# Performance work log

Hardware: AMD Instinct MI355X
Metric: run time of the kernel (lower is better)

## Reference

```python
import jax, jax.numpy as jnp
import numpy as np

N_NODES = 50000
N_EDGES = 800000
LEAKY_SLOPE = 0.25


def setup_inputs() -> dict:
    key = jax.random.key(0)
    ks = jax.random.split(key, 12)
    in_dim, h = 512, [256, 256, 128, 128]
    x = jax.random.normal(ks[0], (N_NODES, in_dim), dtype=jnp.float32)
    row = jax.random.randint(ks[1], (N_EDGES,), 0, N_NODES, dtype=jnp.int32)
    col = jax.random.randint(ks[2], (N_EDGES,), 0, N_NODES, dtype=jnp.int32)
    vals = jax.random.uniform(ks[3], (N_EDGES,), dtype=jnp.float32)
    def xavier(k, fan_in, fan_out):
        std = np.sqrt(2.0 / (fan_in + fan_out))
        return jax.random.normal(k, (fan_in, fan_out), dtype=jnp.float32) * std
    W1 = xavier(ks[4], in_dim, h[0]); b1 = jnp.zeros((h[0],), jnp.float32)
    W2 = xavier(ks[5], h[0], h[1]);  b2 = jnp.zeros((h[1],), jnp.float32)
    W3 = xavier(ks[6], h[1], h[2]);  b3 = jnp.zeros((h[2],), jnp.float32)
    W4 = xavier(ks[7], h[2], h[3]);  b4 = jnp.zeros((h[3],), jnp.float32)
    return {"x": x, "row": row, "col": col, "vals": vals,
            "W1": W1, "b1": b1, "W2": W2, "b2": b2,
            "W3": W3, "b3": b3, "W4": W4, "b4": b4}


def _gconv(x, row, col, vals, W, b):
    # support = x @ W  (dense transform), then SpMM: out[i] = sum_e vals[e] * support[col[e]] for row[e]==i
    support = x @ W
    msgs = support[col] * vals[:, None]           # [E, out_dim] gather + edge-weight
    out = jax.ops.segment_sum(msgs, row, num_segments=x.shape[0])  # scatter-add
    return out + b


def reference(x, row, col, vals, W1, b1, W2, b2, W3, b3, W4, b4):
    lrelu = lambda t: jnp.where(t >= 0, t, LEAKY_SLOPE * t)
    # dropout is identity in eval mode (deterministic reference)
    h = lrelu(_gconv(x, row, col, vals, W1, b1))
    h = lrelu(_gconv(h, row, col, vals, W2, b2))
    h = lrelu(_gconv(h, row, col, vals, W3, b3))
    h = lrelu(_gconv(h, row, col, vals, W4, b4))
    return h
```

## Files before the change

kernel.cpp:

```cpp
#include <hip/hip_runtime.h>
#include <hip/hip_bf16.h>

#define NN 50000
#define NE 800000
#define LEAKY 0.25f
#define SCAN_NB ((NN + 255) / 256)

typedef __attribute__((ext_vector_type(8))) short bf16x8;
typedef __attribute__((ext_vector_type(8))) ushort u16x8;
typedef __attribute__((ext_vector_type(4))) float f32x4;
typedef unsigned long long ull;

#define AS1 const __attribute__((address_space(1))) void*
#define AS3 __attribute__((address_space(3))) void*

static __device__ __forceinline__ ushort f2bf(float f) {
    union { __hip_bfloat16 h; ushort u; } cv;
    cv.h = __float2bfloat16(f);
    return cv.u;
}
static __device__ __forceinline__ float bf2f(ushort u) {
    union { unsigned u; float f; } cv;
    cv.u = ((unsigned)u) << 16;
    return cv.f;
}

__global__ void cast_bf16_x8(const float4* __restrict__ in, u16x8* __restrict__ out, int n8) {
    int i = blockIdx.x * blockDim.x + threadIdx.x;
    if (i >= n8) return;
    float4 v0 = in[i * 2];
    float4 v1 = in[i * 2 + 1];
    u16x8 o;
    o[0] = f2bf(v0.x); o[1] = f2bf(v0.y); o[2] = f2bf(v0.z); o[3] = f2bf(v0.w);
    o[4] = f2bf(v1.x); o[5] = f2bf(v1.y); o[6] = f2bf(v1.z); o[7] = f2bf(v1.w);
    out[i] = o;
}

__global__ void cast_transpose_all(const float* __restrict__ W1, const float* __restrict__ W2,
                                   const float* __restrict__ W3, const float* __restrict__ W4,
                                   ushort* __restrict__ Wt1, ushort* __restrict__ Wt2,
                                   ushort* __restrict__ Wt3, ushort* __restrict__ Wt4) {
    int idx = blockIdx.x * blockDim.x + threadIdx.x;
    const float* W; ushort* Wt; int K, N, base;
    if (idx < 131072)      { W = W1; Wt = Wt1; K = 512; N = 256; base = 0; }
    else if (idx < 196608) { W = W2; Wt = Wt2; K = 256; N = 256; base = 131072; }
    else if (idx < 229376) { W = W3; Wt = Wt3; K = 256; N = 128; base = 196608; }
    else if (idx < 245760) { W = W4; Wt = Wt4; K = 128; N = 128; base = 229376; }
    else return;
    int l = idx - base;
    int k = l / N, n = l % N;
    Wt[n * K + k] = f2bf(W[l]);
}

template<int BN>
__global__ __launch_bounds__(256) void gemm_bf16(
    const ushort* __restrict__ A, const ushort* __restrict__ Bt,
    ushort* __restrict__ C, int M, int K)
{
    constexpr int NI = BN / 32;
    constexpr int BPASS = BN / 64;
    constexpr int ASZ = 64 * 32;
    constexpr int BSZ = BN * 32;
    __shared__ ushort As[2 * ASZ];
    __shared__ ushort Bs[2 * BSZ];
    const int tid  = threadIdx.x;
    const int lane = tid & 63;
    const int wid  = tid >> 6;
    const int wr = wid >> 1, wc = wid & 1;
    const int m0 = blockIdx.x * 64;

    int ar = m0 + (tid >> 2); if (ar >= M) ar = M - 1;
    const int ccol = (tid & 3) * 8;

    const ushort* gA = A + (size_t)ar * K + ccol;
    const ushort* gB[BPASS];
    #pragma unroll
    for (int p = 0; p < BPASS; ++p)
        gB[p] = Bt + (size_t)(p * 64 + (tid >> 2)) * K + ccol;

    const int fr = lane & 15;
    const int fq = lane >> 4;

    auto STAGE = [&](int buf, int k0) {
        char* lA = (char*)(As + buf * ASZ) + wid * 1024;
        char* lB = (char*)(Bs + buf * BSZ) + wid * 1024;
        __builtin_amdgcn_global_load_lds((AS1)(gA + k0), (AS3)lA, 16, 0, 0);
        #pragma unroll
        for (int p = 0; p < BPASS; ++p)
            __builtin_amdgcn_global_load_lds((AS1)(gB[p] + k0), (AS3)(lB + p * 4096), 16, 0, 0);
    };

    f32x4 acc[2][NI];
    #pragma unroll
    for (int i = 0; i < 2; ++i)
        #pragma unroll
        for (int j = 0; j < NI; ++j)
            acc[i][j] = {0.f, 0.f, 0.f, 0.f};

    STAGE(0, 0);
    const int nk = K >> 5;
    for (int t = 0; t < nk; ++t) {
        const int cur = t & 1;
        __syncthreads();
        if (t + 1 < nk) STAGE(cur ^ 1, (t + 1) << 5);

        const ushort* fragA = As + cur * ASZ + (wr * 32 + fr) * 32 + fq * 8;
        const ushort* fragB = Bs + cur * BSZ + (wc * (BN / 2) + fr) * 32 + fq * 8;
        bf16x8 a[2], b[NI];
        #pragma unroll
        for (int mi = 0; mi < 2; ++mi) a[mi] = *(const bf16x8*)(fragA + mi * 16 * 32);
        #pragma unroll
        for (int ni = 0; ni < NI; ++ni) b[ni] = *(const bf16x8*)(fragB + ni * 16 * 32);
        #pragma unroll
        for (int mi = 0; mi < 2; ++mi)
            #pragma unroll
            for (int ni = 0; ni < NI; ++ni)
                acc[mi][ni] = __builtin_amdgcn_mfma_f32_16x16x32_bf16(a[mi], b[ni], acc[mi][ni], 0, 0, 0);
    }

    #pragma unroll
    for (int mi = 0; mi < 2; ++mi) {
        #pragma unroll
        for (int j = 0; j < 4; ++j) {
            int row = m0 + wr * 32 + mi * 16 + fq * 4 + j;
            if (row >= M) continue;
            #pragma unroll
            for (int ni = 0; ni < NI; ++ni) {
                int colg = wc * (BN / 2) + ni * 16 + fr;
                C[(size_t)row * BN + colg] = f2bf(acc[mi][ni][j]);
            }
        }
    }
}

__global__ void hist_rows(const int* __restrict__ row, int* __restrict__ cnt) {
    int e = blockIdx.x * blockDim.x + threadIdx.x;
    if (e < NE) atomicAdd(&cnt[row[e]], 1);
}

__global__ void scan_bsum(const int* __restrict__ cnt, int* __restrict__ bsum) {
    int i = blockIdx.x * 256 + threadIdx.x;
    int v = (i < NN) ? cnt[i] : 0;
    #pragma unroll
    for (int off = 32; off >= 1; off >>= 1) v += __shfl_down(v, off);
    __shared__ int ws[4];
    if ((threadIdx.x & 63) == 0) ws[threadIdx.x >> 6] = v;
    __syncthreads();
    if (threadIdx.x == 0) bsum[blockIdx.x] = ws[0] + ws[1] + ws[2] + ws[3];
}

__global__ void scan_boff(const int* __restrict__ bsum, int* __restrict__ boff,
                          int* __restrict__ rowptr) {
    __shared__ int s[256];
    int t = threadIdx.x;
    int v = (t < SCAN_NB) ? bsum[t] : 0;
    s[t] = v;
    __syncthreads();
    #pragma unroll
    for (int off = 1; off < 256; off <<= 1) {
        int u = (t >= off) ? s[t - off] : 0;
        __syncthreads();
        s[t] += u;
        __syncthreads();
    }
    if (t < SCAN_NB) boff[t] = s[t] - v;
    if (t == 255) rowptr[NN] = s[255];
}

__global__ void scan_write(const int* __restrict__ cnt, const int* __restrict__ boff,
                           int* __restrict__ rowptr, int* __restrict__ rowcur) {
    __shared__ int s[256];
    int b = blockIdx.x;
    int t = threadIdx.x;
    int i = b * 256 + t;
    int v = (i < NN) ? cnt[i] : 0;
    s[t] = v;
    __syncthreads();
    #pragma unroll
    for (int off = 1; off < 256; off <<= 1) {
        int u = (t >= off) ? s[t - off] : 0;
        __syncthreads();
        s[t] += u;
        __syncthreads();
    }
    if (i < NN) {
        int ex = boff[b] + s[t] - v;
        rowptr[i] = ex;
        rowcur[i] = ex;
    }
}

__global__ void scatter_edges(const int* __restrict__ row, const int* __restrict__ col,
                              const float* __restrict__ vals,
                              int* __restrict__ rowcur,
                              ull* __restrict__ epack) {
    int e = blockIdx.x * blockDim.x + threadIdx.x;
    if (e < NE) {
        int p = atomicAdd(&rowcur[row[e]], 1);
        ull pk = ((ull)__float_as_uint(vals[e]) << 32) | (unsigned)col[e];
        epack[p] = pk;
    }
}

template<int DIM, bool OUT_BF16>
__global__ __launch_bounds__(256) void spmm_gather_bf16(
    const ushort* __restrict__ support,
    const int* __restrict__ rowptr,
    const ull* __restrict__ epack,
    const float* __restrict__ bias,
    void* __restrict__ out) {
    constexpr int LPR = DIM / 8;
    constexpr int RPB = 256 / LPR;
    int r = blockIdx.x * RPB + threadIdx.x / LPR;
    int lane = threadIdx.x % LPR;
    if (r >= NN) return;
    int s = rowptr[r], e = rowptr[r + 1];
    float acc0[8] = {}, acc1[8] = {};
    int i = s;
    for (; i + 3 < e; i += 4) {
        ull p0 = epack[i];
        ull p1 = epack[i + 1];
        ull p2 = epack[i + 2];
        ull p3 = epack[i + 3];
        u16x8 v0 = *((const u16x8*)(support + (size_t)(unsigned)p0 * DIM) + lane);
        u16x8 v1 = *((const u16x8*)(support + (size_t)(unsigned)p1 * DIM) + lane);
        u16x8 v2 = *((const u16x8*)(support + (size_t)(unsigned)p2 * DIM) + lane);
        u16x8 v3 = *((const u16x8*)(support + (size_t)(unsigned)p3 * DIM) + lane);
        float w0 = __uint_as_float((unsigned)(p0 >> 32));
        float w1 = __uint_as_float((unsigned)(p1 >> 32));
        float w2 = __uint_as_float((unsigned)(p2 >> 32));
        float w3 = __uint_as_float((unsigned)(p3 >> 32));
        #pragma unroll
        for (int j = 0; j < 8; ++j) acc0[j] += w0 * bf2f(v0[j]);
        #pragma unroll
        for (int j = 0; j < 8; ++j) acc1[j] += w1 * bf2f(v1[j]);
        #pragma unroll
        for (int j = 0; j < 8; ++j) acc0[j] += w2 * bf2f(v2[j]);
        #pragma unroll
        for (int j = 0; j < 8; ++j) acc1[j] += w3 * bf2f(v3[j]);
    }
    for (; i < e; ++i) {
        ull p0 = epack[i];
        float w0 = __uint_as_float((unsigned)(p0 >> 32));
        u16x8 v0 = *((const u16x8*)(support + (size_t)(unsigned)p0 * DIM) + lane);
        #pragma unroll
        for (int j = 0; j < 8; ++j) acc0[j] += w0 * bf2f(v0[j]);
    }
    const float4 bb0 = ((const float4*)bias)[lane * 2];
    const float4 bb1 = ((const float4*)bias)[lane * 2 + 1];
    float acc[8];
    #pragma unroll
    for (int j = 0; j < 8; ++j) acc[j] = acc0[j] + acc1[j];
    acc[0] += bb0.x; acc[1] += bb0.y; acc[2] += bb0.z; acc[3] += bb0.w;
    acc[4] += bb1.x; acc[5] += bb1.y; acc[6] += bb1.z; acc[7] += bb1.w;
    #pragma unroll
    for (int j = 0; j < 8; ++j) acc[j] = (acc[j] >= 0.f) ? acc[j] : LEAKY * acc[j];
    if (OUT_BF16) {
        ushort4 o0, o1;
        o0.x = f2bf(acc[0]); o0.y = f2bf(acc[1]); o0.z = f2bf(acc[2]); o0.w = f2bf(acc[3]);
        o1.x = f2bf(acc[4]); o1.y = f2bf(acc[5]); o1.z = f2bf(acc[6]); o1.w = f2bf(acc[7]);
        ((ushort4*)out)[(size_t)r * LPR * 2 + lane * 2]     = o0;
        ((ushort4*)out)[(size_t)r * LPR * 2 + lane * 2 + 1] = o1;
    } else {
        float4 f0 = {acc[0], acc[1], acc[2], acc[3]};
        float4 f1 = {acc[4], acc[5], acc[6], acc[7]};
        ((float4*)out)[(size_t)r * LPR * 2 + lane * 2]     = f0;
        ((float4*)out)[(size_t)r * LPR * 2 + lane * 2 + 1] = f1;
    }
}

extern "C" void kernel_launch(void* const* d_in, const int* in_sizes, int n_in,
                              void* d_out, int out_size, void* d_ws, size_t ws_size,
                              hipStream_t stream) {
    const float* x    = (const float*)d_in[0];
    const int*   row  = (const int*)d_in[1];
    const int*   col  = (const int*)d_in[2];
    const float* vals = (const float*)d_in[3];
    const float* W1 = (const float*)d_in[4];  const float* b1 = (const float*)d_in[5];
    const float* W2 = (const float*)d_in[6];  const float* b2 = (const float*)d_in[7];
    const float* W3 = (const float*)d_in[8];  const float* b3 = (const float*)d_in[9];
    const float* W4 = (const float*)d_in[10]; const float* b4 = (const float*)d_in[11];

    ushort* Xb = (ushort*)d_ws;
    ushort* Hb = Xb;
    ushort* S  = Xb + (size_t)NN * 512;
    ushort* Wt1 = S + (size_t)NN * 256;
    ushort* Wt2 = Wt1 + 512 * 256;
    ushort* Wt3 = Wt2 + 256 * 256;
    ushort* Wt4 = Wt3 + 256 * 128;
    int* cnt    = (int*)(Wt4 + 128 * 128);
    int* rowptr = cnt + NN;
    int* rowcur = rowptr + (NN + 1);
    int* pend   = rowcur + (NN + 1);
    ull* epack  = (ull*)pend;
    int* bsum   = (int*)(epack + NE);
    int* boff   = bsum + SCAN_NB;
    float* out  = (float*)d_out;

    {
        int n8 = NN * 512 / 8;
        cast_bf16_x8<<<(n8 + 255) / 256, 256, 0, stream>>>((const float4*)x, (u16x8*)Xb, n8);
        cast_transpose_all<<<(245760 + 255) / 256, 256, 0, stream>>>(W1, W2, W3, W4, Wt1, Wt2, Wt3, Wt4);
    }

    hipMemsetAsync(cnt, 0, NN * sizeof(int), stream);
    hist_rows<<<(NE + 255) / 256, 256, 0, stream>>>(row, cnt);
    scan_bsum<<<SCAN_NB, 256, 0, stream>>>(cnt, bsum);
    scan_boff<<<1, 256, 0, stream>>>(bsum, boff, rowptr);
    scan_write<<<SCAN_NB, 256, 0, stream>>>(cnt, boff, rowptr, rowcur);
    scatter_edges<<<(NE + 255) / 256, 256, 0, stream>>>(row, col, vals, rowcur, epack);

    const int MT64 = (NN + 63) / 64;

    gemm_bf16<256><<<MT64, 256, 0, stream>>>(Xb, Wt1, S, NN, 512);
    spmm_gather_bf16<256, true><<<(NN + 7) / 8, 256, 0, stream>>>(S, rowptr, epack, b1, Hb);
    gemm_bf16<256><<<MT64, 256, 0, stream>>>(Hb, Wt2, S, NN, 256);
    spmm_gather_bf16<256, true><<<(NN + 7) / 8, 256, 0, stream>>>(S, rowptr, epack, b2, Hb);
    gemm_bf16<128><<<MT64, 256, 0, stream>>>(Hb, Wt3, S, NN, 256);
    spmm_gather_bf16<128, true><<<(NN + 15) / 16, 256, 0, stream>>>(S, rowptr, epack, b3, Hb);
    gemm_bf16<128><<<MT64, 256, 0, stream>>>(Hb, Wt4, S, NN, 128);
    spmm_gather_bf16<128, false><<<(NN + 15) / 16, 256, 0, stream>>>(S, rowptr, epack, b4, out);
}
```

Baseline: 373.6 us.

## Fuse fp32-to-bf16 input cast into first-layer GEMM and use nontemporal accesses

Removes the separate kernel that converts the 50000x512 fp32 input to bf16. The first GEMM now loads fp32 rows directly, converts them in registers and writes bf16 into shared memory, saving a full write and re-read of the converted matrix. Edge-pack stores/loads and the SpMM output stores become nontemporal to reduce cache pollution. The register-staged A load is synchronous rather than async-to-LDS and doubles A read bytes per tile, which may reduce GEMM overlap.

```diff
diff --git a/kernel.cpp b/kernel.cpp
--- a/kernel.cpp
+++ b/kernel.cpp
@@ -23,17 +23,6 @@
     union { unsigned u; float f; } cv;
     cv.u = ((unsigned)u) << 16;
     return cv.f;
-}
-
-__global__ void cast_bf16_x8(const float4* __restrict__ in, u16x8* __restrict__ out, int n8) {
-    int i = blockIdx.x * blockDim.x + threadIdx.x;
-    if (i >= n8) return;
-    float4 v0 = in[i * 2];
-    float4 v1 = in[i * 2 + 1];
-    u16x8 o;
-    o[0] = f2bf(v0.x); o[1] = f2bf(v0.y); o[2] = f2bf(v0.z); o[3] = f2bf(v0.w);
-    o[4] = f2bf(v1.x); o[5] = f2bf(v1.y); o[6] = f2bf(v1.z); o[7] = f2bf(v1.w);
-    out[i] = o;
 }
 
 __global__ void cast_transpose_all(const float* __restrict__ W1, const float* __restrict__ W2,
@@ -50,6 +39,92 @@
     int l = idx - base;
     int k = l / N, n = l % N;
     Wt[n * K + k] = f2bf(W[l]);
+}
+
+__global__ __launch_bounds__(256) void gemm_l1(
+    const float* __restrict__ X, const ushort* __restrict__ Bt,
+    ushort* __restrict__ C, int M, int K)
+{
+    constexpr int BN = 256, NI = 8, BPASS = 4;
+    constexpr int ASZ = 64 * 32, BSZ = BN * 32;
+    __shared__ ushort As[2 * ASZ];
+    __shared__ ushort Bs[2 * BSZ];
+    const int tid  = threadIdx.x;
+    const int lane = tid & 63;
+    const int wid  = tid >> 6;
+    const int wr = wid >> 1, wc = wid & 1;
+    const int m0 = blockIdx.x * 64;
+
+    int ar = m0 + (tid >> 2); if (ar >= M) ar = M - 1;
+    const int ccol = (tid & 3) * 8;
+
+    const float* gX = X + (size_t)ar * K + ccol;
+    const ushort* gB[BPASS];
+    #pragma unroll
+    for (int p = 0; p < BPASS; ++p)
+        gB[p] = Bt + (size_t)(p * 64 + (tid >> 2)) * K + ccol;
+
+    const int fr = lane & 15;
+    const int fq = lane >> 4;
+    ushort* aslot = As + (tid >> 2) * 32 + (tid & 3) * 8;
+
+    auto STAGE_B = [&](int buf, int k0) {
+        char* lB = (char*)(Bs + buf * BSZ) + wid * 1024;
+        #pragma unroll
+        for (int p = 0; p < BPASS; ++p)
+            __builtin_amdgcn_global_load_lds((AS1)(gB[p] + k0), (AS3)(lB + p * 4096), 16, 0, 0);
+    };
+    auto STAGE_A = [&](int buf, int k0) {
+        float4 u0 = *(const float4*)(gX + k0);
+        float4 u1 = *(const float4*)(gX + k0 + 4);
+        u16x8 o;
+        o[0] = f2bf(u0.x); o[1] = f2bf(u0.y); o[2] = f2bf(u0.z); o[3] = f2bf(u0.w);
+        o[4] = f2bf(u1.x); o[5] = f2bf(u1.y); o[6] = f2bf(u1.z); o[7] = f2bf(u1.w);
+        *(u16x8*)(aslot + buf * ASZ) = o;
+    };
+
+    f32x4 acc[2][NI];
+    #pragma unroll
+    for (int i = 0; i < 2; ++i)
+        #pragma unroll
+        for (int j = 0; j < NI; ++j)
+            acc[i][j] = {0.f, 0.f, 0.f, 0.f};
+
+    STAGE_B(0, 0);
+    STAGE_A(0, 0);
+    const int nk = K >> 5;
+    for (int t = 0; t < nk; ++t) {
+        const int cur = t & 1;
+        __syncthreads();
+        if (t + 1 < nk) { STAGE_B(cur ^ 1, (t + 1) << 5); STAGE_A(cur ^ 1, (t + 1) << 5); }
+
+        const ushort* fragA = As + cur * ASZ + (wr * 32 + fr) * 32 + fq * 8;
+        const ushort* fragB = Bs + cur * BSZ + (wc * (BN / 2) + fr) * 32 + fq * 8;
+        bf16x8 a[2], b[NI];
+        #pragma unroll
+        for (int mi = 0; mi < 2; ++mi) a[mi] = *(const bf16x8*)(fragA + mi * 16 * 32);
+        #pragma unroll
+        for (int ni = 0; ni < NI; ++ni) b[ni] = *(const bf16x8*)(fragB + ni * 16 * 32);
+        #pragma unroll
+        for (int mi = 0; mi < 2; ++mi)
+            #pragma unroll
+            for (int ni = 0; ni < NI; ++ni)
+                acc[mi][ni] = __builtin_amdgcn_mfma_f32_16x16x32_bf16(a[mi], b[ni], acc[mi][ni], 0, 0, 0);
+    }
+
+    #pragma unroll
+    for (int mi = 0; mi < 2; ++mi) {
+        #pragma unroll
+        for (int j = 0; j < 4; ++j) {
+            int row = m0 + wr * 32 + mi * 16 + fq * 4 + j;
+            if (row >= M) continue;
+            #pragma unroll
+            for (int ni = 0; ni < NI; ++ni) {
+                int colg = wc * (BN / 2) + ni * 16 + fr;
+                C[(size_t)row * BN + colg] = f2bf(acc[mi][ni][j]);
+            }
+        }
+    }
 }
 
 template<int BN>
@@ -198,7 +273,7 @@
     if (e < NE) {
         int p = atomicAdd(&rowcur[row[e]], 1);
         ull pk = ((ull)__float_as_uint(vals[e]) << 32) | (unsigned)col[e];
-        epack[p] = pk;
+        __builtin_nontemporal_store(pk, &epack[p]);
     }
 }
 
@@ -218,10 +293,10 @@
     float acc0[8] = {}, acc1[8] = {};
     int i = s;
     for (; i + 3 < e; i += 4) {
-        ull p0 = epack[i];
-        ull p1 = epack[i + 1];
-        ull p2 = epack[i + 2];
-        ull p3 = epack[i + 3];
+        ull p0 = __builtin_nontemporal_load(&epack[i]);
+        ull p1 = __builtin_nontemporal_load(&epack[i + 1]);
+        ull p2 = __builtin_nontemporal_load(&epack[i + 2]);
+        ull p3 = __builtin_nontemporal_load(&epack[i + 3]);
         u16x8 v0 = *((const u16x8*)(support + (size_t)(unsigned)p0 * DIM) + lane);
         u16x8 v1 = *((const u16x8*)(support + (size_t)(unsigned)p1 * DIM) + lane);
         u16x8 v2 = *((const u16x8*)(support + (size_t)(unsigned)p2 * DIM) + lane);
@@ -240,7 +315,7 @@
         for (int j = 0; j < 8; ++j) acc1[j] += w3 * bf2f(v3[j]);
     }
     for (; i < e; ++i) {
-        ull p0 = epack[i];
+        ull p0 = __builtin_nontemporal_load(&epack[i]);
         float w0 = __uint_as_float((unsigned)(p0 >> 32));
         u16x8 v0 = *((const u16x8*)(support + (size_t)(unsigned)p0 * DIM) + lane);
         #pragma unroll
@@ -256,16 +331,16 @@
     #pragma unroll
     for (int j = 0; j < 8; ++j) acc[j] = (acc[j] >= 0.f) ? acc[j] : LEAKY * acc[j];
     if (OUT_BF16) {
-        ushort4 o0, o1;
-        o0.x = f2bf(acc[0]); o0.y = f2bf(acc[1]); o0.z = f2bf(acc[2]); o0.w = f2bf(acc[3]);
-        o1.x = f2bf(acc[4]); o1.y = f2bf(acc[5]); o1.z = f2bf(acc[6]); o1.w = f2bf(acc[7]);
-        ((ushort4*)out)[(size_t)r * LPR * 2 + lane * 2]     = o0;
-        ((ushort4*)out)[(size_t)r * LPR * 2 + lane * 2 + 1] = o1;
+        u16x8 ov;
+        #pragma unroll
+        for (int j = 0; j < 8; ++j) ov[j] = f2bf(acc[j]);
+        __builtin_nontemporal_store(ov, (u16x8*)((ushort*)out + (size_t)r * DIM + lane * 8));
     } else {
-        float4 f0 = {acc[0], acc[1], acc[2], acc[3]};
-        float4 f1 = {acc[4], acc[5], acc[6], acc[7]};
-        ((float4*)out)[(size_t)r * LPR * 2 + lane * 2]     = f0;
-        ((float4*)out)[(size_t)r * LPR * 2 + lane * 2 + 1] = f1;
+        f32x4 f0 = {acc[0], acc[1], acc[2], acc[3]};
+        f32x4 f1 = {acc[4], acc[5], acc[6], acc[7]};
+        float* op = (float*)out + (size_t)r * DIM + lane * 8;
+        __builtin_nontemporal_store(f0, (f32x4*)op);
+        __builtin_nontemporal_store(f1, (f32x4*)(op + 4));
     }
 }
 
@@ -281,9 +356,8 @@
     const float* W3 = (const float*)d_in[8];  const float* b3 = (const float*)d_in[9];
     const float* W4 = (const float*)d_in[10]; const float* b4 = (const float*)d_in[11];
 
-    ushort* Xb = (ushort*)d_ws;
-    ushort* Hb = Xb;
-    ushort* S  = Xb + (size_t)NN * 512;
+    ushort* Hb = (ushort*)d_ws;
+    ushort* S  = Hb + (size_t)NN * 256;
     ushort* Wt1 = S + (size_t)NN * 256;
     ushort* Wt2 = Wt1 + 512 * 256;
     ushort* Wt3 = Wt2 + 256 * 256;
@@ -297,11 +371,7 @@
     int* boff   = bsum + SCAN_NB;
     float* out  = (float*)d_out;
 
-    {
-        int n8 = NN * 512 / 8;
-        cast_bf16_x8<<<(n8 + 255) / 256, 256, 0, stream>>>((const float4*)x, (u16x8*)Xb, n8);
-        cast_transpose_all<<<(245760 + 255) / 256, 256, 0, stream>>>(W1, W2, W3, W4, Wt1, Wt2, Wt3, Wt4);
-    }
+    cast_transpose_all<<<(245760 + 255) / 256, 256, 0, stream>>>(W1, W2, W3, W4, Wt1, Wt2, Wt3, Wt4);
 
     hipMemsetAsync(cnt, 0, NN * sizeof(int), stream);
     hist_rows<<<(NE + 255) / 256, 256, 0, stream>>>(row, cnt);
@@ -312,7 +382,7 @@
 
     const int MT64 = (NN + 63) / 64;
 
-    gemm_bf16<256><<<MT64, 256, 0, stream>>>(Xb, Wt1, S, NN, 512);
+    gemm_l1<<<MT64, 256, 0, stream>>>(x, Wt1, S, NN, 512);
     spmm_gather_bf16<256, true><<<(NN + 7) / 8, 256, 0, stream>>>(S, rowptr, epack, b1, Hb);
     gemm_bf16<256><<<MT64, 256, 0, stream>>>(Hb, Wt2, S, NN, 256);
     spmm_gather_bf16<256, true><<<(NN + 7) / 8, 256, 0, stream>>>(S, rowptr, epack, b2, Hb);
```

After: 392.4 us. 1.05x slower.
